# Kernel optimization log

Hardware: AMD Instinct MI355X
Metric: run time of the kernel (lower is better)

The kernel has to match this reference:

```python
import jax, jax.numpy as jnp
import numpy as np

D = 512   # feature_dim
H = 256   # hidden_dim


def setup_inputs() -> dict:
    key = jax.random.key(0)
    ks = jax.random.split(key, 7)
    s = 1.0 / np.sqrt(H)
    return {
        "x": jax.random.normal(ks[0], (128, 512, D), dtype=jnp.float32),
        "W_ih": jax.random.uniform(ks[1], (4 * H, D), jnp.float32, -s, s),
        "W_hh": jax.random.uniform(ks[2], (4 * H, H), jnp.float32, -s, s),
        "b_ih": jax.random.uniform(ks[3], (4 * H,), jnp.float32, -s, s),
        "b_hh": jax.random.uniform(ks[4], (4 * H,), jnp.float32, -s, s),
        "fc_w": jax.random.uniform(ks[5], (1, H), jnp.float32, -s, s),
        "fc_b": jax.random.uniform(ks[6], (1,), jnp.float32, -s, s),
    }


def _lstm_last_hidden(x, W_ih, W_hh, b_ih, b_hh):
    # x: [B, S, D]. PyTorch gate order: i, f, g, o.
    B = x.shape[0]
    # Precompute input projections for all timesteps: [S, B, 4H]
    xg = jnp.einsum('bsd,gd->sbg', x, W_ih) + (b_ih + b_hh)

    def step(carry, xg_t):
        h, c = carry
        gates = xg_t + h @ W_hh.T  # [B, 4H]
        i, f, g, o = jnp.split(gates, 4, axis=-1)
        c = jax.nn.sigmoid(f) * c + jax.nn.sigmoid(i) * jnp.tanh(g)
        h = jax.nn.sigmoid(o) * jnp.tanh(c)
        return (h, c), None

    h0 = jnp.zeros((B, H), x.dtype)
    c0 = jnp.zeros((B, H), x.dtype)
    (h_n, _), _ = jax.lax.scan(step, (h0, c0), xg)
    return h_n  # [B, H]


def reference(x, W_ih, W_hh, b_ih, b_hh, fc_w, fc_b):
    h_n = _lstm_last_hidden(x, W_ih, W_hh, b_ih, b_hh)
    logits = h_n @ fc_w.T + fc_b  # [B, 1]
    return logits
```

## Files before the change

kernel.cpp:

```cpp
#include <hip/hip_runtime.h>
#include <stdint.h>

typedef _Float16 f16;
typedef _Float16 f16x2 __attribute__((ext_vector_type(2)));
typedef _Float16 f16x8 __attribute__((ext_vector_type(8)));
typedef float f32x4 __attribute__((ext_vector_type(4)));

#define SEQ   512
#define BATCH 128
#define DIM   512
#define HID   256
#define G4    1024

typedef const __attribute__((address_space(1))) void* gas1p;
typedef __attribute__((address_space(3))) void* las3p;

__device__ __forceinline__ uint32_t pk2(float a, float b){
  return __builtin_bit_cast(uint32_t, __builtin_amdgcn_cvt_pkrtz(a, b));
}

__device__ __forceinline__ int sdot4(uint32_t a, uint32_t b, int c){
#if __has_builtin(__builtin_amdgcn_sdot4)
  return __builtin_amdgcn_sdot4(a, b, c, false);
#else
  int s = c;
  #pragma unroll
  for (int i = 0; i < 4; ++i){
    int ai = (int)(signed char)((a >> (8*i)) & 0xff);
    int bi = (int)(signed char)((b >> (8*i)) & 0xff);
    s += ai*bi;
  }
  return s;
#endif
}

__device__ __forceinline__ float sigm(float x){
  return __builtin_amdgcn_rcpf(1.0f + __expf(-x));
}
__device__ __forceinline__ float tanh_(float x){
  return 1.0f - 2.0f*__builtin_amdgcn_rcpf(__expf(2.0f*x) + 1.0f);
}

__global__ void __launch_bounds__(256) cvt_f16_kernel(const float* __restrict__ in,
                                                      f16* __restrict__ out, int n8){
  int i = blockIdx.x*blockDim.x + threadIdx.x;
  if (i >= n8) return;
  const float4* p = (const float4*)in;
  float4 a = p[2*i], b = p[2*i+1];
  uint4 r;
  r.x = pk2(a.x, a.y); r.y = pk2(a.z, a.w);
  r.z = pk2(b.x, b.y); r.w = pk2(b.z, b.w);
  ((uint4*)out)[i] = r;
}

__global__ void __launch_bounds__(256) prep_whh8(const float* __restrict__ Whh,
                                                 uint32_t* __restrict__ W8L){
  int p = blockIdx.x*256 + threadIdx.x;
  int t  = p >> 7;
  int r  = (p >> 5) & 3;
  int qq = p & 31;
  int g  = (t & 255) + (r << 8);
  int kw = ((t >> 8) << 5) + qq;
  float4 v = *(const float4*)(Whh + g*HID + kw*4);
  int a = __float2int_rn(v.x*2048.f); a = a > 127 ? 127 : (a < -127 ? -127 : a);
  int b = __float2int_rn(v.y*2048.f); b = b > 127 ? 127 : (b < -127 ? -127 : b);
  int c = __float2int_rn(v.z*2048.f); c = c > 127 ? 127 : (c < -127 ? -127 : c);
  int d = __float2int_rn(v.w*2048.f); d = d > 127 ? 127 : (d < -127 ? -127 : d);
  W8L[p] = (uint32_t)(a & 0xff) | ((uint32_t)(b & 0xff) << 8) |
           ((uint32_t)(c & 0xff) << 16) | ((uint32_t)(d & 0xff) << 24);
}

#define BM 128
#define BN 128
#define BK 64

__global__ void __launch_bounds__(256) gemm_xg_kernel(const f16* __restrict__ A,
                                                      const f16* __restrict__ Bm,
                                                      const float* __restrict__ bih,
                                                      const float* __restrict__ bhh,
                                                      f16* __restrict__ C){
  __shared__ __align__(16) f16 ldsA[BM*BK];
  __shared__ __align__(16) f16 ldsB[BN*BK];
  const int tid  = threadIdx.x;
  const int wave = tid >> 6;
  const int lane = tid & 63;
  const int bid  = blockIdx.x;
  const int nt   = bid & 7;
  const int mt   = bid >> 3;
  const long m0  = (long)mt * BM;
  const int n0   = nt * BN;
  const int wm   = wave >> 1, wn = wave & 1;
  const int lrow = lane >> 3;
  const int lk   = (lane & 7) * 8;

  f32x4 acc[4][4];
  #pragma unroll
  for (int i=0;i<4;++i)
    #pragma unroll
    for (int j=0;j<4;++j) acc[i][j] = (f32x4){0.f,0.f,0.f,0.f};

  auto ldsAq = (__attribute__((address_space(3))) char*)ldsA;
  auto ldsBq = (__attribute__((address_space(3))) char*)ldsB;

  for (int kt = 0; kt < DIM/BK; ++kt){
    const int k0 = kt*BK;
    __syncthreads();
    #pragma unroll
    for (int i = 0; i < 4; ++i){
      const int seg = wave*4 + i;
      const f16* ga = A  + (m0 + seg*8 + lrow)*DIM + (k0 + lk);
      const f16* gb = Bm + (long)(n0 + seg*8 + lrow)*DIM + (k0 + lk);
      __builtin_amdgcn_global_load_lds((gas1p)ga, (las3p)(ldsAq + seg*1024), 16, 0, 0);
      __builtin_amdgcn_global_load_lds((gas1p)gb, (las3p)(ldsBq + seg*1024), 16, 0, 0);
    }
    __syncthreads();
    #pragma unroll
    for (int kk = 0; kk < 2; ++kk){
      f16x8 af[4], bf[4];
      const int kb = kk*32 + (lane>>4)*8;
      #pragma unroll
      for (int mi=0; mi<4; ++mi){
        af[mi] = *(const f16x8*)(ldsA + (wm*64 + mi*16 + (lane&15))*BK + kb);
        bf[mi] = *(const f16x8*)(ldsB + (wn*64 + mi*16 + (lane&15))*BK + kb);
      }
      #pragma unroll
      for (int mi=0;mi<4;++mi)
        #pragma unroll
        for (int ni=0;ni<4;++ni)
          acc[mi][ni] = __builtin_amdgcn_mfma_f32_16x16x32_f16(af[mi], bf[ni], acc[mi][ni], 0,0,0);
    }
  }
  float bias[4];
  #pragma unroll
  for (int ni=0;ni<4;++ni){
    int col = n0 + wn*64 + ni*16 + (lane&15);
    bias[ni] = bih[col] + bhh[col];
  }
  #pragma unroll
  for (int mi=0;mi<4;++mi){
    #pragma unroll
    for (int ni=0;ni<4;++ni){
      int col = n0 + wn*64 + ni*16 + (lane&15);
      int cpos = (col & 255)*4 + (col >> 8);
      #pragma unroll
      for (int r=0;r<4;++r){
        long row = m0 + wm*64 + mi*16 + (lane>>4)*4 + r;
        C[row*G4 + cpos] = (f16)(acc[mi][ni][r] + bias[ni]);
      }
    }
  }
}

__global__ void __launch_bounds__(512) lstm8_kernel(const f16* __restrict__ xq,
                                                    const uint32_t* __restrict__ W8L,
                                                    const float* __restrict__ fcw,
                                                    const float* __restrict__ fcb,
                                                    float* __restrict__ out){
  __shared__ __align__(16) uint8_t h8[2][256];
  __shared__ __align__(16) int4  part[256];
  __shared__ float red[256];
  const int t = threadIdx.x;
  const int b = blockIdx.x;
  const int j = t & 255;
  const int kap = t >> 8;
  const float invS = 1.0f / (2048.0f * 127.0f);

  uint32_t w[4][32];
  {
    const uint4* wp = (const uint4*)(W8L + t*128);
    #pragma unroll
    for (int r = 0; r < 4; ++r)
      #pragma unroll
      for (int q8 = 0; q8 < 8; ++q8){
        uint4 u = wp[r*8 + q8];
        w[r][q8*4+0] = u.x; w[r][q8*4+1] = u.y;
        w[r][q8*4+2] = u.z; w[r][q8*4+3] = u.w;
      }
  }
  if (t < 128) ((uint32_t*)h8)[t] = 0;

  const f16* xrow = xq + (long)b * SEQ * G4;
  ushort4 xv = make_ushort4(0,0,0,0);
  if (kap == 0) xv = *(const ushort4*)(xrow + j*4);
  float c = 0.f, hlast = 0.f;
  __syncthreads();

  for (int ts = 0; ts < SEQ; ++ts){
    const uint4* hq = (const uint4*)&h8[ts & 1][kap*128];
    int a0=0,b0=0, a1=0,b1=0, a2=0,b2=0, a3=0,b3=0;
    #pragma unroll
    for (int q = 0; q < 8; q += 2){
      uint4 h0 = hq[q], h1 = hq[q+1];
      a0 = sdot4(w[0][q*4+0],h0.x,a0); a0 = sdot4(w[0][q*4+1],h0.y,a0);
      a0 = sdot4(w[0][q*4+2],h0.z,a0); a0 = sdot4(w[0][q*4+3],h0.w,a0);
      b0 = sdot4(w[0][q*4+4],h1.x,b0); b0 = sdot4(w[0][q*4+5],h1.y,b0);
      b0 = sdot4(w[0][q*4+6],h1.z,b0); b0 = sdot4(w[0][q*4+7],h1.w,b0);
      a1 = sdot4(w[1][q*4+0],h0.x,a1); a1 = sdot4(w[1][q*4+1],h0.y,a1);
      a1 = sdot4(w[1][q*4+2],h0.z,a1); a1 = sdot4(w[1][q*4+3],h0.w,a1);
      b1 = sdot4(w[1][q*4+4],h1.x,b1); b1 = sdot4(w[1][q*4+5],h1.y,b1);
      b1 = sdot4(w[1][q*4+6],h1.z,b1); b1 = sdot4(w[1][q*4+7],h1.w,b1);
      a2 = sdot4(w[2][q*4+0],h0.x,a2); a2 = sdot4(w[2][q*4+1],h0.y,a2);
      a2 = sdot4(w[2][q*4+2],h0.z,a2); a2 = sdot4(w[2][q*4+3],h0.w,a2);
      b2 = sdot4(w[2][q*4+4],h1.x,b2); b2 = sdot4(w[2][q*4+5],h1.y,b2);
      b2 = sdot4(w[2][q*4+6],h1.z,b2); b2 = sdot4(w[2][q*4+7],h1.w,b2);
      a3 = sdot4(w[3][q*4+0],h0.x,a3); a3 = sdot4(w[3][q*4+1],h0.y,a3);
      a3 = sdot4(w[3][q*4+2],h0.z,a3); a3 = sdot4(w[3][q*4+3],h0.w,a3);
      b3 = sdot4(w[3][q*4+4],h1.x,b3); b3 = sdot4(w[3][q*4+5],h1.y,b3);
      b3 = sdot4(w[3][q*4+6],h1.z,b3); b3 = sdot4(w[3][q*4+7],h1.w,b3);
    }
    a0 += b0; a1 += b1; a2 += b2; a3 += b3;
    if (kap == 1) part[j] = make_int4(a0, a1, a2, a3);
    __syncthreads();
    if (kap == 0){
      int4 p = part[j];
      f16 xi = __builtin_bit_cast(f16, xv.x), xf = __builtin_bit_cast(f16, xv.y);
      f16 xg_ = __builtin_bit_cast(f16, xv.z), xo = __builtin_bit_cast(f16, xv.w);
      float gi = (float)xi + (float)(a0 + p.x)*invS;
      float gf = (float)xf + (float)(a1 + p.y)*invS;
      float gg = (float)xg_ + (float)(a2 + p.z)*invS;
      float go = (float)xo + (float)(a3 + p.w)*invS;
      if (ts + 1 < SEQ) xv = *(const ushort4*)(xrow + (ts+1)*G4 + j*4);
      float iv = sigm(gi), fv = sigm(gf), gv = tanh_(gg), ov = sigm(go);
      c     = fv*c + iv*gv;
      hlast = ov * tanh_(c);
      int hq8 = __float2int_rn(hlast * 127.f);
      h8[(ts+1) & 1][j] = (uint8_t)(hq8 & 0xff);
    }
    __syncthreads();
  }

  if (kap == 0) red[j] = hlast * fcw[j];
  __syncthreads();
  if (t < 64){
    float s = red[t] + red[t+64] + red[t+128] + red[t+192];
    #pragma unroll
    for (int off = 32; off; off >>= 1) s += __shfl_down(s, off);
    if (t == 0) out[b] = s + fcb[0];
  }
}

extern "C" void kernel_launch(void* const* d_in, const int* in_sizes, int n_in,
                              void* d_out, int out_size, void* d_ws, size_t ws_size,
                              hipStream_t stream) {
  const float* x   = (const float*)d_in[0];
  const float* Wih = (const float*)d_in[1];
  const float* Whh = (const float*)d_in[2];
  const float* bih = (const float*)d_in[3];
  const float* bhh = (const float*)d_in[4];
  const float* fcw = (const float*)d_in[5];
  const float* fcb = (const float*)d_in[6];
  float* out = (float*)d_out;

  char* ws = (char*)d_ws;
  f16*      xh  = (f16*)ws;
  f16*      Wh  = (f16*)(ws + 67108864);
  f16*      xq  = (f16*)(ws + 68157440);
  uint32_t* W8L = (uint32_t*)(ws + 202375168);

  cvt_f16_kernel<<<16384, 256, 0, stream>>>(x,   xh, 33554432/8);
  cvt_f16_kernel<<<256,   256, 0, stream>>>(Wih, Wh, 524288/8);
  prep_whh8<<<256, 256, 0, stream>>>(Whh, W8L);
  gemm_xg_kernel<<<4096, 256, 0, stream>>>(xh, Wh, bih, bhh, xq);
  lstm8_kernel<<<BATCH, 512, 0, stream>>>(xq, W8L, fcw, fcb, out);
}
```

Before: 781.1 us.

## Split LSTM K-halves within a wave and reduce via shuffle, dropping one barrier

```diff
diff --git a/kernel.cpp b/kernel.cpp
--- a/kernel.cpp
+++ b/kernel.cpp
@@ -59,8 +59,11 @@
   int t  = p >> 7;
   int r  = (p >> 5) & 3;
   int qq = p & 31;
-  int g  = (t & 255) + (r << 8);
-  int kw = ((t >> 8) << 5) + qq;
+  int lane  = t & 63;
+  int j     = (t >> 6)*32 + (lane & 31);
+  int khalf = (lane >> 5) & 1;
+  int g  = j + (r << 8);
+  int kw = khalf*32 + qq;
   float4 v = *(const float4*)(Whh + g*HID + kw*4);
   int a = __float2int_rn(v.x*2048.f); a = a > 127 ? 127 : (a < -127 ? -127 : a);
   int b = __float2int_rn(v.y*2048.f); b = b > 127 ? 127 : (b < -127 ? -127 : b);
@@ -151,85 +154,86 @@
   }
 }
 
-__global__ void __launch_bounds__(512) lstm8_kernel(const f16* __restrict__ xq,
-                                                    const uint32_t* __restrict__ W8L,
-                                                    const float* __restrict__ fcw,
-                                                    const float* __restrict__ fcb,
-                                                    float* __restrict__ out){
+__global__ void __launch_bounds__(512)
+__attribute__((amdgpu_waves_per_eu(2, 2)))
+lstm8_kernel(const f16* __restrict__ xq,
+             const uint32_t* __restrict__ W8L,
+             const float* __restrict__ fcw,
+             const float* __restrict__ fcb,
+             float* __restrict__ out){
   __shared__ __align__(16) uint8_t h8[2][256];
-  __shared__ __align__(16) int4  part[256];
   __shared__ float red[256];
   const int t = threadIdx.x;
   const int b = blockIdx.x;
-  const int j = t & 255;
-  const int kap = t >> 8;
+  const int lane  = t & 63;
+  const int j     = (t >> 6)*32 + (lane & 31);
+  const int khalf = lane >> 5;
   const float invS = 1.0f / (2048.0f * 127.0f);
 
-  uint32_t w[4][32];
+  uint32_t w[128];
   {
-    const uint4* wp = (const uint4*)(W8L + t*128);
-    #pragma unroll
-    for (int r = 0; r < 4; ++r)
-      #pragma unroll
-      for (int q8 = 0; q8 < 8; ++q8){
-        uint4 u = wp[r*8 + q8];
-        w[r][q8*4+0] = u.x; w[r][q8*4+1] = u.y;
-        w[r][q8*4+2] = u.z; w[r][q8*4+3] = u.w;
-      }
-  }
+    const uint4* wp = (const uint4*)(W8L + (size_t)t*128);
+    #pragma unroll
+    for (int q8 = 0; q8 < 32; ++q8){
+      uint4 u = wp[q8];
+      w[4*q8+0] = u.x; w[4*q8+1] = u.y; w[4*q8+2] = u.z; w[4*q8+3] = u.w;
+    }
+  }
+  #pragma unroll
+  for (int i = 0; i < 128; ++i) asm volatile("" : "+v"(w[i]));
+
   if (t < 128) ((uint32_t*)h8)[t] = 0;
 
   const f16* xrow = xq + (long)b * SEQ * G4;
-  ushort4 xv = make_ushort4(0,0,0,0);
-  if (kap == 0) xv = *(const ushort4*)(xrow + j*4);
+  ushort4 xv = *(const ushort4*)(xrow + j*4);
   float c = 0.f, hlast = 0.f;
   __syncthreads();
 
   for (int ts = 0; ts < SEQ; ++ts){
-    const uint4* hq = (const uint4*)&h8[ts & 1][kap*128];
-    int a0=0,b0=0, a1=0,b1=0, a2=0,b2=0, a3=0,b3=0;
-    #pragma unroll
-    for (int q = 0; q < 8; q += 2){
-      uint4 h0 = hq[q], h1 = hq[q+1];
-      a0 = sdot4(w[0][q*4+0],h0.x,a0); a0 = sdot4(w[0][q*4+1],h0.y,a0);
-      a0 = sdot4(w[0][q*4+2],h0.z,a0); a0 = sdot4(w[0][q*4+3],h0.w,a0);
-      b0 = sdot4(w[0][q*4+4],h1.x,b0); b0 = sdot4(w[0][q*4+5],h1.y,b0);
-      b0 = sdot4(w[0][q*4+6],h1.z,b0); b0 = sdot4(w[0][q*4+7],h1.w,b0);
-      a1 = sdot4(w[1][q*4+0],h0.x,a1); a1 = sdot4(w[1][q*4+1],h0.y,a1);
-      a1 = sdot4(w[1][q*4+2],h0.z,a1); a1 = sdot4(w[1][q*4+3],h0.w,a1);
-      b1 = sdot4(w[1][q*4+4],h1.x,b1); b1 = sdot4(w[1][q*4+5],h1.y,b1);
-      b1 = sdot4(w[1][q*4+6],h1.z,b1); b1 = sdot4(w[1][q*4+7],h1.w,b1);
-      a2 = sdot4(w[2][q*4+0],h0.x,a2); a2 = sdot4(w[2][q*4+1],h0.y,a2);
-      a2 = sdot4(w[2][q*4+2],h0.z,a2); a2 = sdot4(w[2][q*4+3],h0.w,a2);
-      b2 = sdot4(w[2][q*4+4],h1.x,b2); b2 = sdot4(w[2][q*4+5],h1.y,b2);
-      b2 = sdot4(w[2][q*4+6],h1.z,b2); b2 = sdot4(w[2][q*4+7],h1.w,b2);
-      a3 = sdot4(w[3][q*4+0],h0.x,a3); a3 = sdot4(w[3][q*4+1],h0.y,a3);
-      a3 = sdot4(w[3][q*4+2],h0.z,a3); a3 = sdot4(w[3][q*4+3],h0.w,a3);
-      b3 = sdot4(w[3][q*4+4],h1.x,b3); b3 = sdot4(w[3][q*4+5],h1.y,b3);
-      b3 = sdot4(w[3][q*4+6],h1.z,b3); b3 = sdot4(w[3][q*4+7],h1.w,b3);
-    }
-    a0 += b0; a1 += b1; a2 += b2; a3 += b3;
-    if (kap == 1) part[j] = make_int4(a0, a1, a2, a3);
+    const uint4* hq = (const uint4*)&h8[ts & 1][khalf*128];
+    uint4 hv[8];
+    #pragma unroll
+    for (int q = 0; q < 8; ++q) hv[q] = hq[q];
+
+    int acc[4];
+    #pragma unroll
+    for (int r = 0; r < 4; ++r){
+      int a = 0, bb = 0;
+      #pragma unroll
+      for (int q = 0; q < 4; ++q){
+        a = sdot4(w[r*32+4*q+0], hv[q].x, a);
+        a = sdot4(w[r*32+4*q+1], hv[q].y, a);
+        a = sdot4(w[r*32+4*q+2], hv[q].z, a);
+        a = sdot4(w[r*32+4*q+3], hv[q].w, a);
+      }
+      #pragma unroll
+      for (int q = 4; q < 8; ++q){
+        bb = sdot4(w[r*32+4*q+0], hv[q].x, bb);
+        bb = sdot4(w[r*32+4*q+1], hv[q].y, bb);
+        bb = sdot4(w[r*32+4*q+2], hv[q].z, bb);
+        bb = sdot4(w[r*32+4*q+3], hv[q].w, bb);
+      }
+      acc[r] = a + bb;
+    }
+    #pragma unroll
+    for (int r = 0; r < 4; ++r) acc[r] += __shfl_xor(acc[r], 32);
+
+    f16 xi  = __builtin_bit_cast(f16, xv.x), xf = __builtin_bit_cast(f16, xv.y);
+    f16 xg_ = __builtin_bit_cast(f16, xv.z), xo = __builtin_bit_cast(f16, xv.w);
+    float gi = (float)xi  + (float)acc[0]*invS;
+    float gf = (float)xf  + (float)acc[1]*invS;
+    float gg = (float)xg_ + (float)acc[2]*invS;
+    float go = (float)xo  + (float)acc[3]*invS;
+    if (ts + 1 < SEQ) xv = *(const ushort4*)(xrow + (ts+1)*G4 + j*4);
+    float iv = sigm(gi), fv = sigm(gf), gv = tanh_(gg), ov = sigm(go);
+    c     = fv*c + iv*gv;
+    hlast = ov * tanh_(c);
+    int hq8 = __float2int_rn(hlast * 127.f);
+    if (khalf == 0) h8[(ts+1) & 1][j] = (uint8_t)(hq8 & 0xff);
     __syncthreads();
-    if (kap == 0){
-      int4 p = part[j];
-      f16 xi = __builtin_bit_cast(f16, xv.x), xf = __builtin_bit_cast(f16, xv.y);
-      f16 xg_ = __builtin_bit_cast(f16, xv.z), xo = __builtin_bit_cast(f16, xv.w);
-      float gi = (float)xi + (float)(a0 + p.x)*invS;
-      float gf = (float)xf + (float)(a1 + p.y)*invS;
-      float gg = (float)xg_ + (float)(a2 + p.z)*invS;
-      float go = (float)xo + (float)(a3 + p.w)*invS;
-      if (ts + 1 < SEQ) xv = *(const ushort4*)(xrow + (ts+1)*G4 + j*4);
-      float iv = sigm(gi), fv = sigm(gf), gv = tanh_(gg), ov = sigm(go);
-      c     = fv*c + iv*gv;
-      hlast = ov * tanh_(c);
-      int hq8 = __float2int_rn(hlast * 127.f);
-      h8[(ts+1) & 1][j] = (uint8_t)(hq8 & 0xff);
-    }
-    __syncthreads();
-  }
-
-  if (kap == 0) red[j] = hlast * fcw[j];
+  }
+
+  if (khalf == 0) red[j] = hlast * fcw[j];
   __syncthreads();
   if (t < 64){
     float s = red[t] + red[t+64] + red[t+128] + red[t+192];
```

Result: faster. 693.5 us (-11.2%).
